# Optimization experiments

Hardware: AMD Instinct MI355X
Metric: run time of the kernel (lower is better)

## Reference

```python
import jax, jax.numpy as jnp
import numpy as np

B, CIN, H, W = 8, 128, 64, 64
COUT = 128
UP = 2
KH = KW = 2 * UP  # 4
K = KH * KW       # 16
HO, WO = H - KH + 1, W - KW + 1  # stride=1, padding=0 (defaults actually used)


def setup_inputs() -> dict:
    key = jax.random.key(0)
    k1, k2, k3, k4, k5 = jax.random.split(key, 5)
    inp = jax.random.normal(k1, (B, CIN, H, W), jnp.float32)
    offset = jax.random.normal(k2, (B, 2 * K, HO, WO), jnp.float32)
    mask = jax.random.uniform(k3, (B, K, HO, WO), jnp.float32)
    fan_in = CIN * KH * KW
    bound = 1.0 / np.sqrt(fan_in)  # kaiming_uniform(a=sqrt(5)) bound
    weight = jax.random.uniform(k4, (COUT, CIN, KH, KW), jnp.float32, -bound, bound)
    bias = jax.random.uniform(k5, (COUT,), jnp.float32, -bound, bound)
    return {"input": inp, "offset": offset, "mask": mask, "weight": weight, "bias": bias}


def _deform_conv(inp, offset, mask, weight, bias):
    # modulated deformable conv, groups=1, stride=1, pad=0, dilation=1
    b, cin, h, w = inp.shape
    ho, wo = offset.shape[2], offset.shape[3]
    k = mask.shape[1]
    off = offset.reshape(b, k, 2, ho, wo)
    dy, dx = off[:, :, 0], off[:, :, 1]              # [b,k,ho,wo]

    ki, kj = jnp.meshgrid(jnp.arange(KH), jnp.arange(KW), indexing="ij")
    ki = ki.reshape(k).astype(inp.dtype)
    kj = kj.reshape(k).astype(inp.dtype)

    # sampling coords: base output pixel + kernel tap + learned offset
    y = dy + ki[None, :, None, None] + jnp.arange(ho, dtype=inp.dtype)[None, None, :, None]
    x = dx + kj[None, :, None, None] + jnp.arange(wo, dtype=inp.dtype)[None, None, None, :]

    y0f = jnp.floor(y)
    x0f = jnp.floor(x)
    wy = y - y0f                                     # [b,k,ho,wo]
    wx = x - x0f
    y0 = y0f.astype(jnp.int32)
    x0 = x0f.astype(jnp.int32)

    inp_flat = inp.reshape(b, cin, h * w)

    def gather(yy, xx):
        valid = (yy >= 0) & (yy < h) & (xx >= 0) & (xx < w)
        idx = (jnp.clip(yy, 0, h - 1) * w + jnp.clip(xx, 0, w - 1)).reshape(b, -1)
        v = jnp.take_along_axis(inp_flat, idx[:, None, :], axis=2)
        v = v.reshape(b, cin, k, ho, wo)
        return v * valid[:, None].astype(inp.dtype)

    v00 = gather(y0, x0)
    v01 = gather(y0, x0 + 1)
    v10 = gather(y0 + 1, x0)
    v11 = gather(y0 + 1, x0 + 1)

    wy = wy[:, None]  # [b,1,k,ho,wo]
    wx = wx[:, None]
    sampled = (v00 * (1 - wy) * (1 - wx) + v01 * (1 - wy) * wx
               + v10 * wy * (1 - wx) + v11 * wy * wx)
    sampled = sampled * mask[:, None]                # mask modulation

    # weight is flipped in forward: weight.flip(-1, -2)
    w_flip = weight[:, :, ::-1, ::-1].reshape(weight.shape[0], cin, k)
    out = jnp.einsum("bckhw,ock->bohw", sampled, w_flip)
    return out + bias[None, :, None, None]


def reference(input, offset, mask, weight, bias):
    return _deform_conv(input, offset, mask, weight, bias)
```

## Files before the change

kernel.cpp:

```cpp
#include <hip/hip_runtime.h>
#include <hip/hip_bf16.h>

#define B_    8
#define CIN   128
#define H_    64
#define W_    64
#define COUT  128
#define K_    16
#define HO    61
#define WO    61
#define HW_   (HO * WO)

typedef short bf16x8 __attribute__((ext_vector_type(8)));
typedef short s16x4  __attribute__((ext_vector_type(4)));
typedef float f32x4  __attribute__((ext_vector_type(4)));
typedef float f32x4u __attribute__((ext_vector_type(4), aligned(4)));

#define B2F(s) __uint_as_float(((unsigned int)(unsigned short)(s)) << 16)

__global__ __launch_bounds__(256) void prep_all(const float* __restrict__ inp,
                                                const float* __restrict__ w,
                                                __hip_bfloat16* __restrict__ T,
                                                __hip_bfloat16* __restrict__ A2) {
    const int t = threadIdx.x;
    if (blockIdx.x < 512) {
        __shared__ float ld[64][129];
        const int b  = blockIdx.x >> 6;
        const int sb = (blockIdx.x & 63) << 6;
        const float* src = inp + ((size_t)b << 19);
        #pragma unroll
        for (int i = 0; i < 8; ++i) {
            int j  = i * 256 + t;
            int c  = j >> 4;
            int s4 = (j & 15) << 2;
            f32x4u v = *(const f32x4u*)(const void*)(src + ((size_t)c << 12) + sb + s4);
            #pragma unroll
            for (int q = 0; q < 4; ++q) ld[s4 + q][c] = v[q];
        }
        __syncthreads();
        __hip_bfloat16* dst = T + (((size_t)b << 12) + sb) * 128;
        #pragma unroll
        for (int i = 0; i < 8; ++i) {
            int j  = i * 256 + t;
            int s  = j >> 5;
            int c4 = (j & 31) << 2;
            s16x4 v;
            #pragma unroll
            for (int q = 0; q < 4; ++q) {
                __hip_bfloat16 hh = __float2bfloat16(ld[s][c4 + q]);
                v[q] = *reinterpret_cast<const short*>(&hh);
            }
            *(s16x4*)(void*)(dst + (size_t)s * 128 + c4) = v;
        }
    } else {
        int gid  = (blockIdx.x - 512) * 256 + t;
        int lane = gid & 63;
        int it   = (gid >> 6) & 63;
        int blk  = gid >> 12;
        int o    = blk * 16 + (lane & 15);
        int kk   = it * 32 + (lane >> 4) * 8;
        int k    = kk >> 7;
        int c0   = kk & 127;
        const float* srcw = w + (((size_t)(o << 7) + c0) << 4) + (15 - k);
        __hip_bfloat16* dst = A2 + (size_t)gid * 8;
        #pragma unroll
        for (int j = 0; j < 8; ++j)
            dst[j] = __float2bfloat16(srcw[j << 4]);
    }
}

__global__ __launch_bounds__(512, 4) void deform_gather(
        const __hip_bfloat16* __restrict__ T, const float* __restrict__ off,
        const float* __restrict__ msk, const __hip_bfloat16* __restrict__ A2,
        const float* __restrict__ bias, float* __restrict__ out) {

    __shared__ __align__(16) __hip_bfloat16 Bs[2][64 * 128];
    __shared__ float pw[4][1024];
    __shared__ int   pb[2][1024];

    const int t   = threadIdx.x;
    const int bid = blockIdx.x;
    const int b   = bid & 7;
    const int ho  = bid >> 3;

    #pragma unroll
    for (int ii = 0; ii < 2; ++ii) {
        const int idx = ii * 512 + t;
        const int px  = idx & 63;
        const int k   = idx >> 6;
        const bool pvalid = (px < WO);
        const int wo_c = pvalid ? px : (WO - 1);
        const int r    = ho * WO + wo_c;
        const int ki = k >> 2, kj = k & 3;
        const size_t offb = (size_t)b * (2 * K_ * HW_);
        float dy = off[offb + (size_t)(2 * k)     * HW_ + r];
        float dx = off[offb + (size_t)(2 * k + 1) * HW_ + r];
        float mm = msk[(size_t)b * (K_ * HW_) + (size_t)k * HW_ + r];
        if (!pvalid) mm = 0.0f;

        float y   = dy + (float)(ki + ho);
        float x   = dx + (float)(kj + wo_c);
        float y0f = floorf(y), x0f = floorf(x);
        float wy  = y - y0f,   wx  = x - x0f;
        int y0 = (int)y0f, x0 = (int)x0f;
        int y1 = y0 + 1,   x1 = x0 + 1;

        float wy0v = (1.0f - wy) * ((y0 >= 0 && y0 < H_) ? mm : 0.0f);
        float wy1v = wy          * ((y1 >= 0 && y1 < H_) ? mm : 0.0f);
        int cy0 = min(max(y0, 0), H_ - 1), cy1 = min(max(y1, 0), H_ - 1);

        float wx0v = (1.0f - wx) * ((x0 >= 0 && x0 < W_) ? 1.0f : 0.0f);
        float wx1v = wx          * ((x1 >= 0 && x1 < W_) ? 1.0f : 0.0f);
        int xb = min(max(x0, 0), W_ - 2);
        int tsh = x0 - xb;
        float a0 = (tsh == 0) ? wx0v : ((tsh == -1) ? wx1v : 0.0f);
        float a1 = (tsh == 0) ? wx1v : ((tsh ==  1) ? wx0v : 0.0f);

        pw[0][idx] = wy0v * a0;  pw[1][idx] = wy0v * a1;
        pw[2][idx] = wy1v * a0;  pw[3][idx] = wy1v * a1;
        pb[0][idx] = (cy0 * W_ + xb) << 7;
        pb[1][idx] = (cy1 * W_ + xb) << 7;
    }
    __syncthreads();

    const int lane = t & 63;
    const int wv   = t >> 6;
    const int p_g  = lane >> 2;
    const int mrow = lane & 15;
    const int quad = lane >> 4;
    const __hip_bfloat16* Tb = T + ((size_t)b << 19);

    int rowU[2], cbU[2];
    #pragma unroll
    for (int i = 0; i < 2; ++i) {
        const int u = (wv << 1) + i;
        rowU[i] = ((u >> 2) << 4) + p_g;
        cbU[i]  = ((u & 3) << 5) + ((lane & 3) << 3);
    }

    f32x4 accA = {0.f,0.f,0.f,0.f}, accB = {0.f,0.f,0.f,0.f};
    f32x4 accC = {0.f,0.f,0.f,0.f}, accD = {0.f,0.f,0.f,0.f};

    bf16x8 cU[2][4];
    float  wtU[2][4];
    int    swzU[2];

    auto uget = [&](int qp) {
        #pragma unroll
        for (int i = 0; i < 2; ++i) {
            const int pidx = (qp << 6) + rowU[i];
            wtU[i][0] = pw[0][pidx]; wtU[i][1] = pw[1][pidx];
            wtU[i][2] = pw[2][pidx]; wtU[i][3] = pw[3][pidx];
            const __hip_bfloat16* p0 = Tb + pb[0][pidx] + cbU[i];
            const __hip_bfloat16* p1 = Tb + pb[1][pidx] + cbU[i];
            cU[i][0] = *(const bf16x8*)(const void*)(p0);
            cU[i][1] = *(const bf16x8*)(const void*)(p0 + 128);
            cU[i][2] = *(const bf16x8*)(const void*)(p1);
            cU[i][3] = *(const bf16x8*)(const void*)(p1 + 128);
            swzU[i] = (rowU[i] << 7) + ((cbU[i] + (rowU[i] << 3)) & 127);
        }
    };

    auto ucomb = [&](int bb_) {
        #pragma unroll
        for (int i = 0; i < 2; ++i) {
            bf16x8 v;
            #pragma unroll
            for (int q = 0; q < 8; ++q) {
                float s = wtU[i][0] * B2F(cU[i][0][q]) + wtU[i][1] * B2F(cU[i][1][q])
                        + wtU[i][2] * B2F(cU[i][2][q]) + wtU[i][3] * B2F(cU[i][3][q]);
                __hip_bfloat16 hh = __float2bfloat16(s);
                v[q] = *reinterpret_cast<const short*>(&hh);
            }
            *(bf16x8*)(void*)(&Bs[bb_][swzU[i]]) = v;
        }
    };

    bf16x8 avR[4];
    auto loadA = [&](int qp) {
        #pragma unroll
        for (int s_ = 0; s_ < 4; ++s_) {
            avR[s_] = *(const bf16x8*)(const void*)(
                A2 + ((size_t)((wv * 64 + qp * 4 + s_) * 64 + lane) << 3));
        }
    };

    auto mfma_exec = [&](int qp) {
        const int bb_ = qp & 1;
        #pragma unroll
        for (int s_ = 0; s_ < 4; ++s_) {
            const int base = (s_ << 5) + (quad << 3);
            const int r0 = mrow,      i0 = (r0 << 7) + ((base + (r0 << 3)) & 127);
            const int r1 = 16 + mrow, i1 = (r1 << 7) + ((base + (r1 << 3)) & 127);
            const int r2 = 32 + mrow, i2 = (r2 << 7) + ((base + (r2 << 3)) & 127);
            const int r3 = 48 + mrow, i3 = (r3 << 7) + ((base + (r3 << 3)) & 127);
            bf16x8 b0 = *(const bf16x8*)(const void*)(&Bs[bb_][i0]);
            bf16x8 b1 = *(const bf16x8*)(const void*)(&Bs[bb_][i1]);
            bf16x8 b2 = *(const bf16x8*)(const void*)(&Bs[bb_][i2]);
            bf16x8 b3 = *(const bf16x8*)(const void*)(&Bs[bb_][i3]);
            accA = __builtin_amdgcn_mfma_f32_16x16x32_bf16(avR[s_], b0, accA, 0, 0, 0);
            accB = __builtin_amdgcn_mfma_f32_16x16x32_bf16(avR[s_], b1, accB, 0, 0, 0);
            accC = __builtin_amdgcn_mfma_f32_16x16x32_bf16(avR[s_], b2, accC, 0, 0, 0);
            accD = __builtin_amdgcn_mfma_f32_16x16x32_bf16(avR[s_], b3, accD, 0, 0, 0);
        }
    };

    uget(0);
    ucomb(0);
    loadA(0);
    __syncthreads();

    #pragma unroll 1
    for (int qp = 1; qp < 16; ++qp) {
        uget(qp);
        __builtin_amdgcn_s_setprio(1);
        mfma_exec(qp - 1);
        __builtin_amdgcn_s_setprio(0);
        loadA(qp);
        ucomb(qp & 1);
        __syncthreads();
    }
    mfma_exec(15);

    #pragma unroll
    for (int pg = 0; pg < 4; ++pg) {
        const int px = (pg << 4) + mrow;
        if (px < WO) {
            const size_t outb = (size_t)b * (COUT * HW_) + (size_t)(ho * WO + px);
            const f32x4 a = (pg == 0) ? accA : (pg == 1) ? accB
                          : (pg == 2) ? accC : accD;
            #pragma unroll
            for (int jj = 0; jj < 4; ++jj) {
                const int o = wv * 16 + quad * 4 + jj;
                out[outb + (size_t)o * HW_] = a[jj] + bias[o];
            }
        }
    }
}

extern "C" void kernel_launch(void* const* d_in, const int* in_sizes, int n_in,
                              void* d_out, int out_size, void* d_ws, size_t ws_size,
                              hipStream_t stream) {
    const float* inp  = (const float*)d_in[0];
    const float* off  = (const float*)d_in[1];
    const float* msk  = (const float*)d_in[2];
    const float* wgt  = (const float*)d_in[3];
    const float* bias = (const float*)d_in[4];
    float* out = (float*)d_out;

    __hip_bfloat16* A2 = (__hip_bfloat16*)d_ws;
    __hip_bfloat16* T  = (__hip_bfloat16*)((char*)d_ws + (1 << 20));

    prep_all<<<640, 256, 0, stream>>>(inp, wgt, T, A2);

    int nblk = B_ * HO;
    deform_gather<<<nblk, 512, 0, stream>>>(T, off, msk, A2, bias, out);
}
```

Measured before the change: 114.2 us.

## Prefetch gathers two stages ahead, XOR-swizzle LDS, and packed bilinear combine

Splits the gathered corner registers into even and odd sets so the global loads for step qp+1 are issued one full iteration before they are combined, giving the gather latency more room to hide behind MFMA work. The loop is unrolled by two with explicit tail handling. The LDS swizzle changes from an additive rotate to an XOR pattern, and the bilinear combine now decodes bf16 pairs from 32-bit words and uses float2 vector math. The cost is doubled corner-value register usage, which may reduce occupancy.

```diff
diff --git a/kernel.cpp b/kernel.cpp
--- a/kernel.cpp
+++ b/kernel.cpp
@@ -13,10 +13,10 @@
 
 typedef short bf16x8 __attribute__((ext_vector_type(8)));
 typedef short s16x4  __attribute__((ext_vector_type(4)));
+typedef int   s32x4  __attribute__((ext_vector_type(4)));
 typedef float f32x4  __attribute__((ext_vector_type(4)));
+typedef float f32x2  __attribute__((ext_vector_type(2)));
 typedef float f32x4u __attribute__((ext_vector_type(4), aligned(4)));
-
-#define B2F(s) __uint_as_float(((unsigned int)(unsigned short)(s)) << 16)
 
 __global__ __launch_bounds__(256) void prep_all(const float* __restrict__ inp,
                                                 const float* __restrict__ w,
@@ -130,53 +130,65 @@
     const int quad = lane >> 4;
     const __hip_bfloat16* Tb = T + ((size_t)b << 19);
 
-    int rowU[2], cbU[2];
+    int rowU[2], cbU[2], swzU[2];
     #pragma unroll
     for (int i = 0; i < 2; ++i) {
         const int u = (wv << 1) + i;
         rowU[i] = ((u >> 2) << 4) + p_g;
         cbU[i]  = ((u & 3) << 5) + ((lane & 3) << 3);
+        swzU[i] = (rowU[i] << 7) + (((cbU[i] >> 3) ^ (rowU[i] & 7)) << 3);
     }
 
     f32x4 accA = {0.f,0.f,0.f,0.f}, accB = {0.f,0.f,0.f,0.f};
     f32x4 accC = {0.f,0.f,0.f,0.f}, accD = {0.f,0.f,0.f,0.f};
 
-    bf16x8 cU[2][4];
-    float  wtU[2][4];
-    int    swzU[2];
-
-    auto uget = [&](int qp) {
+    s32x4 cE[2][4], cO[2][4];
+    bf16x8 avR[4];
+
+    auto uget = [&](int qp, s32x4 (&cv)[2][4]) {
         #pragma unroll
         for (int i = 0; i < 2; ++i) {
             const int pidx = (qp << 6) + rowU[i];
-            wtU[i][0] = pw[0][pidx]; wtU[i][1] = pw[1][pidx];
-            wtU[i][2] = pw[2][pidx]; wtU[i][3] = pw[3][pidx];
             const __hip_bfloat16* p0 = Tb + pb[0][pidx] + cbU[i];
             const __hip_bfloat16* p1 = Tb + pb[1][pidx] + cbU[i];
-            cU[i][0] = *(const bf16x8*)(const void*)(p0);
-            cU[i][1] = *(const bf16x8*)(const void*)(p0 + 128);
-            cU[i][2] = *(const bf16x8*)(const void*)(p1);
-            cU[i][3] = *(const bf16x8*)(const void*)(p1 + 128);
-            swzU[i] = (rowU[i] << 7) + ((cbU[i] + (rowU[i] << 3)) & 127);
-        }
-    };
-
-    auto ucomb = [&](int bb_) {
+            cv[i][0] = *(const s32x4*)(const void*)(p0);
+            cv[i][1] = *(const s32x4*)(const void*)(p0 + 128);
+            cv[i][2] = *(const s32x4*)(const void*)(p1);
+            cv[i][3] = *(const s32x4*)(const void*)(p1 + 128);
+        }
+    };
+
+    auto ucomb = [&](int qp, const s32x4 (&cv)[2][4]) {
+        const int bb_ = qp & 1;
         #pragma unroll
         for (int i = 0; i < 2; ++i) {
+            const int pidx = (qp << 6) + rowU[i];
+            const float w0 = pw[0][pidx], w1 = pw[1][pidx];
+            const float w2 = pw[2][pidx], w3 = pw[3][pidx];
             bf16x8 v;
             #pragma unroll
-            for (int q = 0; q < 8; ++q) {
-                float s = wtU[i][0] * B2F(cU[i][0][q]) + wtU[i][1] * B2F(cU[i][1][q])
-                        + wtU[i][2] * B2F(cU[i][2][q]) + wtU[i][3] * B2F(cU[i][3][q]);
-                __hip_bfloat16 hh = __float2bfloat16(s);
-                v[q] = *reinterpret_cast<const short*>(&hh);
+            for (int jj = 0; jj < 4; ++jj) {
+                const unsigned a = (unsigned)cv[i][0][jj];
+                const unsigned bq = (unsigned)cv[i][1][jj];
+                const unsigned c = (unsigned)cv[i][2][jj];
+                const unsigned d = (unsigned)cv[i][3][jj];
+                f32x2 va = { __uint_as_float(a << 16),  __uint_as_float(a & 0xffff0000u) };
+                f32x2 vb = { __uint_as_float(bq << 16), __uint_as_float(bq & 0xffff0000u) };
+                f32x2 vc = { __uint_as_float(c << 16),  __uint_as_float(c & 0xffff0000u) };
+                f32x2 vd = { __uint_as_float(d << 16),  __uint_as_float(d & 0xffff0000u) };
+                f32x2 s = va * w0;
+                s += vb * w1;
+                s += vc * w2;
+                s += vd * w3;
+                __hip_bfloat16 h0 = __float2bfloat16(s[0]);
+                __hip_bfloat16 h1 = __float2bfloat16(s[1]);
+                v[2*jj]   = *reinterpret_cast<const short*>(&h0);
+                v[2*jj+1] = *reinterpret_cast<const short*>(&h1);
             }
             *(bf16x8*)(void*)(&Bs[bb_][swzU[i]]) = v;
         }
     };
 
-    bf16x8 avR[4];
     auto loadA = [&](int qp) {
         #pragma unroll
         for (int s_ = 0; s_ < 4; ++s_) {
@@ -187,13 +199,14 @@
 
     auto mfma_exec = [&](int qp) {
         const int bb_ = qp & 1;
+        const int mx = mrow & 7;
         #pragma unroll
         for (int s_ = 0; s_ < 4; ++s_) {
-            const int base = (s_ << 5) + (quad << 3);
-            const int r0 = mrow,      i0 = (r0 << 7) + ((base + (r0 << 3)) & 127);
-            const int r1 = 16 + mrow, i1 = (r1 << 7) + ((base + (r1 << 3)) & 127);
-            const int r2 = 32 + mrow, i2 = (r2 << 7) + ((base + (r2 << 3)) & 127);
-            const int r3 = 48 + mrow, i3 = (r3 << 7) + ((base + (r3 << 3)) & 127);
+            const int colX = ((((s_ << 2) + quad) ^ mx) << 3);
+            const int i0 = (mrow << 7) + colX;
+            const int i1 = ((16 + mrow) << 7) + colX;
+            const int i2 = ((32 + mrow) << 7) + colX;
+            const int i3 = ((48 + mrow) << 7) + colX;
             bf16x8 b0 = *(const bf16x8*)(const void*)(&Bs[bb_][i0]);
             bf16x8 b1 = *(const bf16x8*)(const void*)(&Bs[bb_][i1]);
             bf16x8 b2 = *(const bf16x8*)(const void*)(&Bs[bb_][i2]);
@@ -205,21 +218,35 @@
         }
     };
 
-    uget(0);
-    ucomb(0);
+    uget(0, cE);
+    uget(1, cO);
     loadA(0);
+    ucomb(0, cE);
     __syncthreads();
 
     #pragma unroll 1
-    for (int qp = 1; qp < 16; ++qp) {
-        uget(qp);
+    for (int qq = 1; qq < 15; qq += 2) {
+        uget(qq + 1, cE);
         __builtin_amdgcn_s_setprio(1);
-        mfma_exec(qp - 1);
+        mfma_exec(qq - 1);
         __builtin_amdgcn_s_setprio(0);
-        loadA(qp);
-        ucomb(qp & 1);
+        loadA(qq);
+        ucomb(qq, cO);
         __syncthreads();
-    }
+        uget(qq + 2, cO);
+        __builtin_amdgcn_s_setprio(1);
+        mfma_exec(qq);
+        __builtin_amdgcn_s_setprio(0);
+        loadA(qq + 1);
+        ucomb(qq + 1, cE);
+        __syncthreads();
+    }
+    __builtin_amdgcn_s_setprio(1);
+    mfma_exec(14);
+    __builtin_amdgcn_s_setprio(0);
+    loadA(15);
+    ucomb(15, cO);
+    __syncthreads();
     mfma_exec(15);
 
     #pragma unroll
```

Result: slower. 117.5 us (+2.9%).
